# Kernel tuning notes

Hardware: AMD Instinct MI355X
Metric: run time of the kernel (lower is better)

Reference implementation:

```python
import jax, jax.numpy as jnp
import numpy as np

DIM = 1024
NUM_HEADS = 16
HEAD_DIM = DIM // NUM_HEADS
FF = 4 * DIM
B, T, S = 8, 512, 4096


def setup_inputs() -> dict:
    key = jax.random.key(0)
    ks = jax.random.split(key, 14)
    sc = 1.0 / np.sqrt(DIM)
    inp = {
        "x": jax.random.normal(ks[0], (B, T, DIM), jnp.float32),
        "inp": jax.random.normal(ks[1], (B, S, DIM), jnp.float32),
        # attention projections
        "Wq": jax.random.normal(ks[2], (DIM, DIM), jnp.float32) * sc,
        "bq": jnp.zeros((DIM,), jnp.float32),
        "Wk": jax.random.normal(ks[3], (DIM, DIM), jnp.float32) * sc,
        "bk": jnp.zeros((DIM,), jnp.float32),
        "Wv": jax.random.normal(ks[4], (DIM, DIM), jnp.float32) * sc,
        "bv": jnp.zeros((DIM,), jnp.float32),
        "Wo": jax.random.normal(ks[5], (DIM, DIM), jnp.float32) * sc,
        "bo": jnp.zeros((DIM,), jnp.float32),
        # MLP
        "W1": jax.random.normal(ks[6], (DIM, FF), jnp.float32) * sc,
        "b1": jnp.zeros((FF,), jnp.float32),
        "W2": jax.random.normal(ks[7], (FF, DIM), jnp.float32) * (1.0 / np.sqrt(FF)),
        "b2": jnp.zeros((DIM,), jnp.float32),
    }
    return inp


def _perceiver_layer(x, inp, Wq, bq, Wk, bk, Wv, bv, Wo, bo, W1, b1, W2, b2):
    b, t, _ = x.shape
    s = inp.shape[1]
    q = (x @ Wq + bq).reshape(b, t, NUM_HEADS, HEAD_DIM)
    k = (inp @ Wk + bk).reshape(b, s, NUM_HEADS, HEAD_DIM)
    v = (inp @ Wv + bv).reshape(b, s, NUM_HEADS, HEAD_DIM)
    # [b, h, t, s] score tensor (as in original code)
    attn = jnp.einsum('bthd,bshd->bhts', q, k)
    attn = jax.nn.softmax(attn / jnp.sqrt(jnp.float32(HEAD_DIM)), axis=-1)
    out = jnp.einsum('bhts,bshd->bthd', attn, v).reshape(b, t, DIM)
    attn_out = out @ Wo + bo
    x = x + attn_out
    h = jax.nn.gelu(x @ W1 + b1, approximate=True)  # flax nn.gelu default is tanh approx
    x = x + (h @ W2 + b2)
    return x


def reference(x, inp, Wq, bq, Wk, bk, Wv, bv, Wo, bo, W1, b1, W2, b2):
    return _perceiver_layer(x, inp, Wq, bq, Wk, bk, Wv, bv, Wo, bo, W1, b1, W2, b2)
```

## Files before the change

kernel.cpp:

```cpp
#include <hip/hip_runtime.h>
#include <hip/hip_bf16.h>

#define DIM 1024
#define NHEADS 16
#define HDIM 64
#define FF_ 4096
#define BB 8
#define TT 512
#define SS 4096

typedef __attribute__((ext_vector_type(8))) __bf16 bf16x8;
typedef __attribute__((ext_vector_type(4))) float f32x4;
typedef __attribute__((ext_vector_type(4))) unsigned short us4;

#define SWZ(r, b) ((b) ^ (((r) & 7) << 4))

typedef const __attribute__((address_space(1))) void gvoid_t;
typedef __attribute__((address_space(3))) void lvoid_t;

__device__ __forceinline__ void ldst16(const void* g, void* l) {
  __builtin_amdgcn_global_load_lds((gvoid_t*)g, (lvoid_t*)l, 16, 0, 0);
}

__device__ inline unsigned short f2bf(float f) {
  unsigned u = __float_as_uint(f);
  u += 0x7fff + ((u >> 16) & 1);
  return (unsigned short)(u >> 16);
}

__device__ __forceinline__ unsigned cvt_pk(float lo, float hi) {
  unsigned r;
  asm("v_cvt_pk_bf16_f32 %0, %1, %2" : "=v"(r) : "v"(lo), "v"(hi));
  return r;
}

__global__ void prep_kernel(const float* __restrict__ x,
                            const float* __restrict__ inp,
                            const float* __restrict__ Wq,
                            const float* __restrict__ Wk,
                            const float* __restrict__ Wv,
                            const float* __restrict__ Wo,
                            const float* __restrict__ W1,
                            const float* __restrict__ W2,
                            const float* __restrict__ bk,
                            const float* __restrict__ bv,
                            unsigned short* __restrict__ xb,
                            unsigned short* __restrict__ inpb,
                            unsigned short* __restrict__ Wqt,
                            unsigned short* __restrict__ Wkvt,
                            unsigned short* __restrict__ Wot,
                            unsigned short* __restrict__ W1t,
                            unsigned short* __restrict__ W2t,
                            float* __restrict__ bkv) {
  __shared__ float tile[32][33];
  const int bid = blockIdx.x, tid = threadIdx.x;

  if (bid < 2048) {
    const int n4 = BB * SS * DIM / 4;
    for (int i = bid * 256 + tid; i < n4; i += 2048 * 256) {
      float4 v = ((const float4*)inp)[i];
      uint2 w = {cvt_pk(v.x, v.y), cvt_pk(v.z, v.w)};
      ((uint2*)inpb)[i] = w;
    }
    return;
  }
  if (bid < 2304) {
    const int n4 = BB * TT * DIM / 4;
    for (int i = (bid - 2048) * 256 + tid; i < n4; i += 256 * 256) {
      float4 v = ((const float4*)x)[i];
      uint2 w = {cvt_pk(v.x, v.y), cvt_pk(v.z, v.w)};
      ((uint2*)xb)[i] = w;
    }
    return;
  }
  if (bid < 14592) {
    const float* in;
    unsigned short* outp;
    int R, C, t, tilesx;
    if (bid < 3328)       { in = Wq; outp = Wqt; R = 1024; C = 1024; t = bid - 2304; tilesx = 32; }
    else if (bid < 4352)  { in = Wk; outp = Wkvt; R = 1024; C = 1024; t = bid - 3328; tilesx = 32; }
    else if (bid < 5376)  { in = Wv; outp = Wkvt + 1024 * 1024; R = 1024; C = 1024; t = bid - 4352; tilesx = 32; }
    else if (bid < 6400)  { in = Wo; outp = Wot; R = 1024; C = 1024; t = bid - 5376; tilesx = 32; }
    else if (bid < 10496) { in = W1; outp = W1t; R = 1024; C = 4096; t = bid - 6400; tilesx = 128; }
    else                  { in = W2; outp = W2t; R = 4096; C = 1024; t = bid - 10496; tilesx = 32; }
    int bc = (t % tilesx) * 32, br = (t / tilesx) * 32;
    int tx = tid & 31, ty = tid >> 5;
#pragma unroll
    for (int i = 0; i < 32; i += 8)
      tile[ty + i][tx] = in[(size_t)(br + ty + i) * C + bc + tx];
    __syncthreads();
#pragma unroll
    for (int i = 0; i < 32; i += 8)
      outp[(size_t)(bc + ty + i) * R + br + tx] = f2bf(tile[tx][ty + i]);
    return;
  }
  for (int i = tid; i < 1024; i += 256) {
    bkv[i] = bk[i];
    bkv[1024 + i] = bv[i];
  }
}

template <int EPI>
__global__ __launch_bounds__(256, 3)
void gemm_kernel(const unsigned short* __restrict__ A,
                 const unsigned short* __restrict__ Bt,
                 const float* __restrict__ bias,
                 const float* __restrict__ res,
                 void* __restrict__ Cp,
                 unsigned short* __restrict__ C2,
                 int M, int N, int K) {
  __shared__ char smem[32768];
  char* As = smem;
  char* Bs = smem + 16384;

  const int tid = threadIdx.x;
  const int lane = tid & 63;
  const int wave = tid >> 6;
  const int wm = wave >> 1, wn = wave & 1;

  const int flat = blockIdx.y * gridDim.x + blockIdx.x;
  const int cpx = (gridDim.x * gridDim.y) >> 3;
  const int swz = (flat & 7) * cpx + (flat >> 3);
  const int m0 = (swz / gridDim.x) * 128, n0 = (swz % gridDim.x) * 128;

  f32x4 acc[4][4];
#pragma unroll
  for (int i = 0; i < 4; ++i)
#pragma unroll
    for (int j = 0; j < 4; ++j) acc[i][j] = (f32x4){0.f, 0.f, 0.f, 0.f};

  for (int k0 = 0; k0 < K; k0 += 64) {
    __syncthreads();
#pragma unroll
    for (int i = 0; i < 4; ++i) {
      int ch = (wave * 4 + i) * 64 + lane;
      int r = ch >> 3, c8 = (ch & 7) ^ (r & 7);
      ldst16(A + (size_t)(m0 + r) * K + k0 + c8 * 8, As + (wave * 4 + i) * 1024);
      ldst16(Bt + (size_t)(n0 + r) * K + k0 + c8 * 8, Bs + (wave * 4 + i) * 1024);
    }
    __syncthreads();

#pragma unroll
    for (int kk = 0; kk < 2; ++kk) {
      bf16x8 a[4], b[4];
#pragma unroll
      for (int mi = 0; mi < 4; ++mi) {
        int r = wm * 64 + mi * 16 + (lane & 15);
        a[mi] = *(const bf16x8*)(As + r * 128 + SWZ(r, kk * 64 + (lane >> 4) * 16));
      }
#pragma unroll
      for (int ni = 0; ni < 4; ++ni) {
        int r = wn * 64 + ni * 16 + (lane & 15);
        b[ni] = *(const bf16x8*)(Bs + r * 128 + SWZ(r, kk * 64 + (lane >> 4) * 16));
      }
#pragma unroll
      for (int mi = 0; mi < 4; ++mi)
#pragma unroll
        for (int ni = 0; ni < 4; ++ni)
          acc[mi][ni] = __builtin_amdgcn_mfma_f32_16x16x32_bf16(b[ni], a[mi], acc[mi][ni], 0, 0, 0);
    }
  }

  const int q = lane & 15, g4 = (lane >> 4) * 4;
#pragma unroll
  for (int mi = 0; mi < 4; ++mi) {
    int row = m0 + wm * 64 + mi * 16 + q;
#pragma unroll
    for (int ni = 0; ni < 4; ++ni) {
      int colb = n0 + wn * 64 + ni * 16 + g4;
      float4 bv = *(const float4*)(bias + colb);
      f32x4 v = acc[mi][ni];
      float v0 = v[0] + bv.x, v1 = v[1] + bv.y, v2 = v[2] + bv.z, v3 = v[3] + bv.w;
      if (EPI == 0) {
        uint2 w = {cvt_pk(v0, v1), cvt_pk(v2, v3)};
        *(uint2*)((unsigned short*)Cp + (size_t)row * N + colb) = w;
      } else if (EPI == 1) {
        float o[4] = {v0, v1, v2, v3};
#pragma unroll
        for (int j = 0; j < 4; ++j) {
          float u = 0.7978845608028654f * (o[j] + 0.044715f * o[j] * o[j] * o[j]);
          float e = __expf(2.f * u);
          float th = 1.f - 2.f / (e + 1.f);
          o[j] = 0.5f * o[j] * (1.f + th);
        }
        uint2 w = {cvt_pk(o[0], o[1]), cvt_pk(o[2], o[3])};
        *(uint2*)((unsigned short*)Cp + (size_t)row * N + colb) = w;
      } else {
        float4 r4 = *(const float4*)(res + (size_t)row * N + colb);
        float o0 = v0 + r4.x, o1 = v1 + r4.y, o2 = v2 + r4.z, o3 = v3 + r4.w;
        float4 ov = {o0, o1, o2, o3};
        *(float4*)((float*)Cp + (size_t)row * N + colb) = ov;
        if (EPI == 3) {
          uint2 w = {cvt_pk(o0, o1), cvt_pk(o2, o3)};
          *(uint2*)(C2 + (size_t)row * N + colb) = w;
        }
      }
    }
  }
}

template <int EPI>
__global__ __launch_bounds__(512, 2)
void gemm256(const unsigned short* __restrict__ A,
             const unsigned short* __restrict__ Bt,
             const float* __restrict__ bias,
             void* __restrict__ Cp,
             unsigned short* __restrict__ C2,
             int M, int N, int K) {
  __shared__ char smem[131072];

  const int tid = threadIdx.x, lane = tid & 63, wave = tid >> 6;
  const int q = lane & 15, g = lane >> 4;
  const int wm = wave >> 2, wn = wave & 3;

  const int flat = blockIdx.y * gridDim.x + blockIdx.x;
  const int cpx = (gridDim.x * gridDim.y) >> 3;
  const int swz = (flat & 7) * cpx + (flat >> 3);
  const int m0 = (swz / gridDim.x) * 256, n0 = (swz % gridDim.x) * 256;

  const unsigned short* Arow = A + (size_t)m0 * K;
  const unsigned short* Brow = Bt + (size_t)n0 * K;

  const int r0 = tid >> 3, c0 = ((tid & 7) ^ (r0 & 7)) * 8;
  const int r1 = (tid + 512) >> 3, c1 = (((tid + 512) & 7) ^ (r1 & 7)) * 8;

#define STA(buf, half, kt)                                                     \
  { char* d = smem + (buf) * 32768 + (half) * 16384;                           \
    const unsigned short* s = Arow + (size_t)((half) * 128) * K + (kt) * 64;   \
    ldst16(s + (size_t)r0 * K + c0, d + tid * 16);                             \
    ldst16(s + (size_t)r1 * K + c1, d + 8192 + tid * 16); }
#define STB(buf, half, kt)                                                     \
  { char* d = smem + 65536 + (buf) * 32768 + (half) * 16384;                   \
    const unsigned short* s = Brow + (size_t)((half) * 128) * K + (kt) * 64;   \
    ldst16(s + (size_t)r0 * K + c0, d + tid * 16);                             \
    ldst16(s + (size_t)r1 * K + c1, d + 8192 + tid * 16); }

  f32x4 acc[8][4];
#pragma unroll
  for (int i = 0; i < 8; ++i)
#pragma unroll
    for (int j = 0; j < 4; ++j) acc[i][j] = (f32x4){0.f, 0.f, 0.f, 0.f};

  STA(0, 0, 0); STA(0, 1, 0); STB(0, 0, 0); STB(0, 1, 0);
  STB(1, 0, 1); STB(1, 1, 1);
  asm volatile("s_waitcnt vmcnt(4)" ::: "memory");
  __builtin_amdgcn_s_barrier();

  const int NKT = K >> 6;
  for (int kt = 0; kt < NKT; ++kt) {
    const int cb = kt & 1, nb = cb ^ 1;
    const char* Ab = smem + cb * 32768;
    const char* Bb = smem + 65536 + cb * 32768;
    bf16x8 bfr[4][2];

#pragma unroll
    for (int p = 0; p < 4; ++p) {
      bf16x8 af[2][2];
#pragma unroll
      for (int i = 0; i < 2; ++i)
#pragma unroll
        for (int kk = 0; kk < 2; ++kk) {
          int r = wm * 128 + (2 * p + i) * 16 + q;
          af[i][kk] = *(const bf16x8*)(Ab + r * 128 + SWZ(r, kk * 64 + g * 16));
        }
      if (p == 0) {
#pragma unroll
        for (int nr = 0; nr < 4; ++nr)
#pragma unroll
          for (int kk = 0; kk < 2; ++kk) {
            int r = wn * 64 + nr * 16 + q;
            bfr[nr][kk] = *(const bf16x8*)(Bb + r * 128 + SWZ(r, kk * 64 + g * 16));
          }
      }

      if (p == 0)      { if (kt + 1 < NKT) { STA(nb, 0, kt + 1); STA(nb, 1, kt + 1); } }
      else if (p == 1) { if (kt + 2 < NKT) STB(cb, 0, kt + 2); }
      else if (p == 2) { if (kt + 2 < NKT) STB(cb, 1, kt + 2); }

      __builtin_amdgcn_s_barrier();
      __builtin_amdgcn_s_setprio(1);
#pragma unroll
      for (int i = 0; i < 2; ++i)
#pragma unroll
        for (int nr = 0; nr < 4; ++nr)
#pragma unroll
          for (int kk = 0; kk < 2; ++kk)
            acc[2 * p + i][nr] = __builtin_amdgcn_mfma_f32_16x16x32_bf16(
                bfr[nr][kk], af[i][kk], acc[2 * p + i][nr], 0, 0, 0);
      __builtin_amdgcn_s_setprio(0);

      if (p == 3) {
        if (kt + 2 < NKT) { asm volatile("s_waitcnt vmcnt(4)" ::: "memory"); }
        else              { asm volatile("s_waitcnt vmcnt(0)" ::: "memory"); }
      }
      __builtin_amdgcn_s_barrier();
    }
  }

  const int g4 = g * 4;
#pragma unroll
  for (int mr = 0; mr < 8; ++mr) {
    int row = m0 + wm * 128 + mr * 16 + q;
#pragma unroll
    for (int nr = 0; nr < 4; ++nr) {
      int colb = n0 + wn * 64 + nr * 16 + g4;
      float4 bv = *(const float4*)(bias + colb);
      f32x4 v = acc[mr][nr];
      float v0 = v[0] + bv.x, v1 = v[1] + bv.y, v2 = v[2] + bv.z, v3 = v[3] + bv.w;
      if (EPI == 1) {
        float o[4] = {v0, v1, v2, v3};
#pragma unroll
        for (int j = 0; j < 4; ++j) {
          float u = 0.7978845608028654f * (o[j] + 0.044715f * o[j] * o[j] * o[j]);
          float e = __expf(2.f * u);
          float th = 1.f - 2.f / (e + 1.f);
          o[j] = 0.5f * o[j] * (1.f + th);
        }
        uint2 w = {cvt_pk(o[0], o[1]), cvt_pk(o[2], o[3])};
        *(uint2*)((unsigned short*)Cp + (size_t)row * N + colb) = w;
      } else {
        if (n0 < 1024) {
          uint2 w = {cvt_pk(v0, v1), cvt_pk(v2, v3)};
          *(uint2*)((unsigned short*)Cp + (size_t)row * 1024 + colb) = w;
        } else {
          int b = row >> 12, s = row & 4095;
          int d0 = colb - 1024;
          unsigned short* vt = C2 + ((size_t)b * DIM + d0) * SS + s;
          vt[0] = f2bf(v0);
          vt[SS] = f2bf(v1);
          vt[2 * SS] = f2bf(v2);
          vt[3 * SS] = f2bf(v3);
        }
      }
    }
  }
#undef STA
#undef STB
}

__global__ __launch_bounds__(512, 4)
void attn_kernel4(const unsigned short* __restrict__ Qb,
                  const unsigned short* __restrict__ Kb,
                  const unsigned short* __restrict__ Vt,
                  unsigned short* __restrict__ Ob) {
  __shared__ char smem[81920];

  const int tid = threadIdx.x, lane = tid & 63, wave = tid >> 6;
  const int bid = blockIdx.x;
  const int b = bid & 7, qt = (bid >> 3) & 3, h = bid >> 5;
  const int q0 = qt * 128;
  const int q = lane & 15, g = lane >> 4;

  const int rK = tid >> 3;
  const int cK = (tid & 7) ^ (rK & 7);
  char* const Pw = smem + 65536 + wave * 2048;

  const unsigned short* srcQ = Qb + ((size_t)b * TT + q0) * DIM + h * HDIM;
  const unsigned short* srcK = Kb + (size_t)b * SS * DIM + h * HDIM;
  const unsigned short* srcV = Vt + ((size_t)b * DIM + h * HDIM) * SS;

  {
    int r = tid >> 3, c = (tid & 7) ^ (r & 7);
    ldst16(srcQ + (size_t)r * DIM + c * 8, smem + tid * 16);
    int ch = tid + 512;
    r = ch >> 3; c = (ch & 7) ^ (r & 7);
    ldst16(srcQ + (size_t)r * DIM + c * 8, smem + ch * 16);
  }
  ldst16(srcK + (size_t)rK * DIM + cK * 8, smem + 16384 + tid * 16);
  ldst16(srcV + (size_t)rK * SS + cK * 8, smem + 40960 + tid * 16);
  ldst16(srcK + (size_t)(64 + rK) * DIM + cK * 8, smem + 24576 + tid * 16);
  ldst16(srcV + (size_t)rK * SS + 64 + cK * 8, smem + 49152 + tid * 16);
  asm volatile("s_waitcnt vmcnt(2)" ::: "memory");
  __builtin_amdgcn_s_barrier();

  bf16x8 qf[2];
  {
    int r = wave * 16 + q;
    qf[0] = *(const bf16x8*)(smem + r * 128 + SWZ(r, g * 16));
    qf[1] = *(const bf16x8*)(smem + r * 128 + SWZ(r, 64 + g * 16));
  }

  f32x4 acc[4];
#pragma unroll
  for (int dt = 0; dt < 4; ++dt) acc[dt] = (f32x4){0.f, 0.f, 0.f, 0.f};
  float lsum = 0.f;
  const float CSC = 0.125f * 1.4426950408889634f;

  const int NT = SS / 64;
  int cur = 0, sb = 2;
  for (int t = 0; t < NT; ++t) {
    char* Kc = smem + 16384 + cur * 8192;
    char* Vc = smem + 40960 + cur * 8192;
    if (t + 2 < NT) {
      char* Kn = smem + 16384 + sb * 8192;
      char* Vn = smem + 40960 + sb * 8192;
      ldst16(srcK + (size_t)((t + 2) * 64 + rK) * DIM + cK * 8, Kn + tid * 16);
      ldst16(srcV + (size_t)rK * SS + (t + 2) * 64 + cK * 8, Vn + tid * 16);
    }

    f32x4 st[4];
#pragma unroll
    for (int si = 0; si < 4; ++si) st[si] = (f32x4){0.f, 0.f, 0.f, 0.f};
#pragma unroll
    for (int kk = 0; kk < 2; ++kk)
#pragma unroll
      for (int si = 0; si < 4; ++si) {
        int r = si * 16 + q;
        bf16x8 kf = *(const bf16x8*)(Kc + r * 128 + SWZ(r, kk * 64 + g * 16));
        st[si] = __builtin_amdgcn_mfma_f32_16x16x32_bf16(kf, qf[kk], st[si], 0, 0, 0);
      }

    float rs = 0.f;
#pragma unroll
    for (int si = 0; si < 4; ++si) {
      float p0 = __builtin_amdgcn_exp2f(st[si][0] * CSC);
      float p1 = __builtin_amdgcn_exp2f(st[si][1] * CSC);
      float p2 = __builtin_amdgcn_exp2f(st[si][2] * CSC);
      float p3 = __builtin_amdgcn_exp2f(st[si][3] * CSC);
      rs += (p0 + p1) + (p2 + p3);
      uint2 w = {cvt_pk(p0, p1), cvt_pk(p2, p3)};
      *(uint2*)(Pw + q * 128 + SWZ(q, si * 32 + g * 8)) = w;
    }
    lsum += rs;

#pragma unroll
    for (int kk = 0; kk < 2; ++kk) {
      bf16x8 pb = *(const bf16x8*)(Pw + q * 128 + SWZ(q, kk * 64 + g * 16));
#pragma unroll
      for (int dt = 0; dt < 4; ++dt) {
        int r = dt * 16 + q;
        bf16x8 va = *(const bf16x8*)(Vc + r * 128 + SWZ(r, kk * 64 + g * 16));
        acc[dt] = __builtin_amdgcn_mfma_f32_16x16x32_bf16(va, pb, acc[dt], 0, 0, 0);
      }
    }

    if (t + 2 < NT) { asm volatile("s_waitcnt vmcnt(2)" ::: "memory"); }
    else            { asm volatile("s_waitcnt vmcnt(0)" ::: "memory"); }
    __builtin_amdgcn_s_barrier();
    cur = cur == 2 ? 0 : cur + 1;
    sb  = sb  == 2 ? 0 : sb  + 1;
  }

  lsum += __shfl_xor(lsum, 16);
  lsum += __shfl_xor(lsum, 32);
  float inv = 1.0f / lsum;
#pragma unroll
  for (int dt = 0; dt < 4; ++dt) {
    f32x4 v = acc[dt];
    uint2 w = {cvt_pk(v[0] * inv, v[1] * inv), cvt_pk(v[2] * inv, v[3] * inv)};
    *(uint2*)(Pw + q * 128 + SWZ(q, dt * 32 + g * 8)) = w;
  }
  __builtin_amdgcn_s_waitcnt(0);
  int qr = lane >> 2, cb = (lane & 3) * 32;
  uint4 lo = *(const uint4*)(Pw + qr * 128 + SWZ(qr, cb));
  uint4 hi = *(const uint4*)(Pw + qr * 128 + SWZ(qr, cb + 16));
  size_t ob = ((size_t)b * TT + q0 + wave * 16 + qr) * DIM + h * HDIM + (lane & 3) * 16;
  *(uint4*)(Ob + ob) = lo;
  *(uint4*)(Ob + ob + 8) = hi;
}

extern "C" void kernel_launch(void* const* d_in, const int* in_sizes, int n_in,
                              void* d_out, int out_size, void* d_ws, size_t ws_size,
                              hipStream_t stream) {
  const float* x   = (const float*)d_in[0];
  const float* inp = (const float*)d_in[1];
  const float* Wq  = (const float*)d_in[2];
  const float* bq  = (const float*)d_in[3];
  const float* Wk  = (const float*)d_in[4];
  const float* bk  = (const float*)d_in[5];
  const float* Wv  = (const float*)d_in[6];
  const float* bv  = (const float*)d_in[7];
  const float* Wo  = (const float*)d_in[8];
  const float* bo  = (const float*)d_in[9];
  const float* W1  = (const float*)d_in[10];
  const float* b1  = (const float*)d_in[11];
  const float* W2  = (const float*)d_in[12];
  const float* b2  = (const float*)d_in[13];
  float* out = (float*)d_out;

  char* ws = (char*)d_ws;
  const size_t MB = 1024ull * 1024ull;
  unsigned short* Wqt  = (unsigned short*)(ws + 0 * MB);
  unsigned short* Wkvt = (unsigned short*)(ws + 2 * MB);
  unsigned short* Wot  = (unsigned short*)(ws + 6 * MB);
  unsigned short* W1t  = (unsigned short*)(ws + 8 * MB);
  unsigned short* W2t  = (unsigned short*)(ws + 16 * MB);
  float*          bkv  = (float*)(ws + 24 * MB);
  unsigned short* Qb   = (unsigned short*)(ws + 25 * MB);
  unsigned short* Kb   = (unsigned short*)(ws + 33 * MB);
  float*          x2   = (float*)(ws + 33 * MB);
  unsigned short* x2b  = (unsigned short*)(ws + 49 * MB);
  unsigned short* hb   = (unsigned short*)(ws + 57 * MB);
  unsigned short* Vt   = (unsigned short*)(ws + 97 * MB);
  unsigned short* inpb = (unsigned short*)(ws + 161 * MB);
  unsigned short* xb   = (unsigned short*)(ws + 225 * MB);
  unsigned short* Obf  = (unsigned short*)d_out;

  prep_kernel<<<dim3(14593), 256, 0, stream>>>(x, inp, Wq, Wk, Wv, Wo, W1, W2,
                                               bk, bv, xb, inpb, Wqt, Wkvt,
                                               Wot, W1t, W2t, bkv);

  gemm_kernel<0><<<dim3(8, 32), 256, 0, stream>>>(xb, Wqt, bq, nullptr, Qb, nullptr, BB * TT, DIM, DIM);
  gemm256<2><<<dim3(8, 128), 512, 0, stream>>>(inpb, Wkvt, bkv, Kb, Vt, BB * SS, 2048, DIM);

  attn_kernel4<<<dim3(512), 512, 0, stream>>>(Qb, Kb, Vt, Obf);

  gemm_kernel<3><<<dim3(8, 32), 256, 0, stream>>>(Obf, Wot, bo, x, x2, x2b, BB * TT, DIM, DIM);
  gemm256<1><<<dim3(16, 16), 512, 0, stream>>>(x2b, W1t, b1, hb, nullptr, BB * TT, FF_, DIM);
  gemm_kernel<2><<<dim3(8, 32), 256, 0, stream>>>(hb, W2t, b2, x2, out, nullptr, BB * TT, DIM, FF_);
}
```

Measured before the change: 458.7 us.

## Prefetch GEMM fragments across phases and shrink attention LDS footprint

In gemm256 the A/B register fragments for the next phase (and the next k-tile) are now read from LDS after the current MFMAs, so LDS reads overlap with compute instead of stalling before it. The vmcnt wait is moved earlier to p==2 so the next buffer is ready for the cross-tile prefetch. In the attention kernel Q is loaded directly from global memory into registers instead of being staged through LDS, cutting shared memory from 80KB to 64KB, which may allow more blocks per CU. The cost is higher register pressure in the GEMM, and uncoalesced direct global Q loads.

```diff
diff --git a/kernel.cpp b/kernel.cpp
--- a/kernel.cpp
+++ b/kernel.cpp
@@ -246,38 +246,37 @@
   asm volatile("s_waitcnt vmcnt(4)" ::: "memory");
   __builtin_amdgcn_s_barrier();
 
+  bf16x8 af[2][2], bfr[4][2];
+#pragma unroll
+  for (int i = 0; i < 2; ++i)
+#pragma unroll
+    for (int kk = 0; kk < 2; ++kk) {
+      int r = wm * 128 + i * 16 + q;
+      af[i][kk] = *(const bf16x8*)(smem + r * 128 + SWZ(r, kk * 64 + g * 16));
+    }
+#pragma unroll
+  for (int nr = 0; nr < 4; ++nr)
+#pragma unroll
+    for (int kk = 0; kk < 2; ++kk) {
+      int r = wn * 64 + nr * 16 + q;
+      bfr[nr][kk] = *(const bf16x8*)(smem + 65536 + r * 128 + SWZ(r, kk * 64 + g * 16));
+    }
+
   const int NKT = K >> 6;
   for (int kt = 0; kt < NKT; ++kt) {
     const int cb = kt & 1, nb = cb ^ 1;
     const char* Ab = smem + cb * 32768;
-    const char* Bb = smem + 65536 + cb * 32768;
-    bf16x8 bfr[4][2];
+    const char* An = smem + nb * 32768;
+    const char* Bn = smem + 65536 + nb * 32768;
 
 #pragma unroll
     for (int p = 0; p < 4; ++p) {
-      bf16x8 af[2][2];
-#pragma unroll
-      for (int i = 0; i < 2; ++i)
-#pragma unroll
-        for (int kk = 0; kk < 2; ++kk) {
-          int r = wm * 128 + (2 * p + i) * 16 + q;
-          af[i][kk] = *(const bf16x8*)(Ab + r * 128 + SWZ(r, kk * 64 + g * 16));
-        }
-      if (p == 0) {
-#pragma unroll
-        for (int nr = 0; nr < 4; ++nr)
-#pragma unroll
-          for (int kk = 0; kk < 2; ++kk) {
-            int r = wn * 64 + nr * 16 + q;
-            bfr[nr][kk] = *(const bf16x8*)(Bb + r * 128 + SWZ(r, kk * 64 + g * 16));
-          }
-      }
-
       if (p == 0)      { if (kt + 1 < NKT) { STA(nb, 0, kt + 1); STA(nb, 1, kt + 1); } }
       else if (p == 1) { if (kt + 2 < NKT) STB(cb, 0, kt + 2); }
       else if (p == 2) { if (kt + 2 < NKT) STB(cb, 1, kt + 2); }
 
       __builtin_amdgcn_s_barrier();
+
       __builtin_amdgcn_s_setprio(1);
 #pragma unroll
       for (int i = 0; i < 2; ++i)
@@ -289,11 +288,51 @@
                 bfr[nr][kk], af[i][kk], acc[2 * p + i][nr], 0, 0, 0);
       __builtin_amdgcn_s_setprio(0);
 
-      if (p == 3) {
+      bf16x8 afn[2][2], bfrn[4][2];
+      const bool have_next = (p < 3) || (kt + 1 < NKT);
+      if (p < 3) {
+#pragma unroll
+        for (int i = 0; i < 2; ++i)
+#pragma unroll
+          for (int kk = 0; kk < 2; ++kk) {
+            int r = wm * 128 + (2 * (p + 1) + i) * 16 + q;
+            afn[i][kk] = *(const bf16x8*)(Ab + r * 128 + SWZ(r, kk * 64 + g * 16));
+          }
+      } else if (kt + 1 < NKT) {
+#pragma unroll
+        for (int i = 0; i < 2; ++i)
+#pragma unroll
+          for (int kk = 0; kk < 2; ++kk) {
+            int r = wm * 128 + i * 16 + q;
+            afn[i][kk] = *(const bf16x8*)(An + r * 128 + SWZ(r, kk * 64 + g * 16));
+          }
+#pragma unroll
+        for (int nr = 0; nr < 4; ++nr)
+#pragma unroll
+          for (int kk = 0; kk < 2; ++kk) {
+            int r = wn * 64 + nr * 16 + q;
+            bfrn[nr][kk] = *(const bf16x8*)(Bn + r * 128 + SWZ(r, kk * 64 + g * 16));
+          }
+      }
+
+      if (p == 2) {
         if (kt + 2 < NKT) { asm volatile("s_waitcnt vmcnt(4)" ::: "memory"); }
         else              { asm volatile("s_waitcnt vmcnt(0)" ::: "memory"); }
       }
       __builtin_amdgcn_s_barrier();
+
+      if (have_next) {
+#pragma unroll
+        for (int i = 0; i < 2; ++i)
+#pragma unroll
+          for (int kk = 0; kk < 2; ++kk) af[i][kk] = afn[i][kk];
+        if (p == 3) {
+#pragma unroll
+          for (int nr = 0; nr < 4; ++nr)
+#pragma unroll
+            for (int kk = 0; kk < 2; ++kk) bfr[nr][kk] = bfrn[nr][kk];
+        }
+      }
     }
   }
 
@@ -339,11 +378,11 @@
 }
 
 __global__ __launch_bounds__(512, 4)
-void attn_kernel4(const unsigned short* __restrict__ Qb,
+void attn_kernel5(const unsigned short* __restrict__ Qb,
                   const unsigned short* __restrict__ Kb,
                   const unsigned short* __restrict__ Vt,
                   unsigned short* __restrict__ Ob) {
-  __shared__ char smem[81920];
+  __shared__ char smem[65536];
 
   const int tid = threadIdx.x, lane = tid & 63, wave = tid >> 6;
   const int bid = blockIdx.x;
@@ -353,32 +392,25 @@
 
   const int rK = tid >> 3;
   const int cK = (tid & 7) ^ (rK & 7);
-  char* const Pw = smem + 65536 + wave * 2048;
+  char* const Pw = smem + 49152 + wave * 2048;
 
   const unsigned short* srcQ = Qb + ((size_t)b * TT + q0) * DIM + h * HDIM;
   const unsigned short* srcK = Kb + (size_t)b * SS * DIM + h * HDIM;
   const unsigned short* srcV = Vt + ((size_t)b * DIM + h * HDIM) * SS;
 
+  bf16x8 qf[2];
   {
-    int r = tid >> 3, c = (tid & 7) ^ (r & 7);
-    ldst16(srcQ + (size_t)r * DIM + c * 8, smem + tid * 16);
-    int ch = tid + 512;
-    r = ch >> 3; c = (ch & 7) ^ (r & 7);
-    ldst16(srcQ + (size_t)r * DIM + c * 8, smem + ch * 16);
-  }
-  ldst16(srcK + (size_t)rK * DIM + cK * 8, smem + 16384 + tid * 16);
-  ldst16(srcV + (size_t)rK * SS + cK * 8, smem + 40960 + tid * 16);
-  ldst16(srcK + (size_t)(64 + rK) * DIM + cK * 8, smem + 24576 + tid * 16);
-  ldst16(srcV + (size_t)rK * SS + 64 + cK * 8, smem + 49152 + tid * 16);
+    const unsigned short* qrow = srcQ + (size_t)(wave * 16 + q) * DIM;
+    qf[0] = *(const bf16x8*)(qrow + g * 8);
+    qf[1] = *(const bf16x8*)(qrow + 32 + g * 8);
+  }
+
+  ldst16(srcK + (size_t)rK * DIM + cK * 8, smem + tid * 16);
+  ldst16(srcV + (size_t)rK * SS + cK * 8, smem + 24576 + tid * 16);
+  ldst16(srcK + (size_t)(64 + rK) * DIM + cK * 8, smem + 8192 + tid * 16);
+  ldst16(srcV + (size_t)rK * SS + 64 + cK * 8, smem + 32768 + tid * 16);
   asm volatile("s_waitcnt vmcnt(2)" ::: "memory");
   __builtin_amdgcn_s_barrier();
-
-  bf16x8 qf[2];
-  {
-    int r = wave * 16 + q;
-    qf[0] = *(const bf16x8*)(smem + r * 128 + SWZ(r, g * 16));
-    qf[1] = *(const bf16x8*)(smem + r * 128 + SWZ(r, 64 + g * 16));
-  }
 
   f32x4 acc[4];
 #pragma unroll
@@ -389,11 +421,11 @@
   const int NT = SS / 64;
   int cur = 0, sb = 2;
   for (int t = 0; t < NT; ++t) {
-    char* Kc = smem + 16384 + cur * 8192;
-    char* Vc = smem + 40960 + cur * 8192;
+    char* Kc = smem + cur * 8192;
+    char* Vc = smem + 24576 + cur * 8192;
     if (t + 2 < NT) {
-      char* Kn = smem + 16384 + sb * 8192;
-      char* Vn = smem + 40960 + sb * 8192;
+      char* Kn = smem + sb * 8192;
+      char* Vn = smem + 24576 + sb * 8192;
       ldst16(srcK + (size_t)((t + 2) * 64 + rK) * DIM + cK * 8, Kn + tid * 16);
       ldst16(srcV + (size_t)rK * SS + (t + 2) * 64 + cK * 8, Vn + tid * 16);
     }
@@ -503,7 +535,7 @@
   gemm_kernel<0><<<dim3(8, 32), 256, 0, stream>>>(xb, Wqt, bq, nullptr, Qb, nullptr, BB * TT, DIM, DIM);
   gemm256<2><<<dim3(8, 128), 512, 0, stream>>>(inpb, Wkvt, bkv, Kb, Vt, BB * SS, 2048, DIM);
 
-  attn_kernel4<<<dim3(512), 512, 0, stream>>>(Qb, Kb, Vt, Obf);
+  attn_kernel5<<<dim3(512), 512, 0, stream>>>(Qb, Kb, Vt, Obf);
 
   gemm_kernel<3><<<dim3(8, 32), 256, 0, stream>>>(Obf, Wot, bo, x, x2, x2b, BB * TT, DIM, DIM);
   gemm256<1><<<dim3(16, 16), 512, 0, stream>>>(x2b, W1t, b1, hb, nullptr, BB * TT, FF_, DIM);
```

Result: slower. 476.0 us (+3.8%).

## Give each attention wave two query tiles to reuse K/V fragments

Applied to the files above, without the earlier changes.

The attention kernel now runs 4 waves of 256 threads per block, each wave handling 32 query rows (two 16-row MFMA tiles) instead of 16. Each K and V fragment read from LDS therefore feeds two MFMAs, halving LDS reads per flop, and Q is loaded straight from global memory into registers rather than staged through shared memory. s_setprio is raised around the MFMA sections to favour matrix issue. The cost is more accumulator registers per wave and fewer waves per block to hide latency, with shared memory cut from 80KB to 64KB.

```diff
diff --git a/kernel.cpp b/kernel.cpp
--- a/kernel.cpp
+++ b/kernel.cpp
@@ -338,12 +338,12 @@
 #undef STB
 }
 
-__global__ __launch_bounds__(512, 4)
-void attn_kernel4(const unsigned short* __restrict__ Qb,
+__global__ __launch_bounds__(256, 2)
+void attn_kernel6(const unsigned short* __restrict__ Qb,
                   const unsigned short* __restrict__ Kb,
                   const unsigned short* __restrict__ Vt,
                   unsigned short* __restrict__ Ob) {
-  __shared__ char smem[81920];
+  __shared__ char smem[65536];
 
   const int tid = threadIdx.x, lane = tid & 63, wave = tid >> 6;
   const int bid = blockIdx.x;
@@ -351,112 +351,146 @@
   const int q0 = qt * 128;
   const int q = lane & 15, g = lane >> 4;
 
-  const int rK = tid >> 3;
-  const int cK = (tid & 7) ^ (rK & 7);
-  char* const Pw = smem + 65536 + wave * 2048;
+  const int rA = tid >> 3;
+  const int cA = (tid & 7) ^ (rA & 7);
+  char* const Pw = smem + 49152 + wave * 4096;
 
   const unsigned short* srcQ = Qb + ((size_t)b * TT + q0) * DIM + h * HDIM;
   const unsigned short* srcK = Kb + (size_t)b * SS * DIM + h * HDIM;
   const unsigned short* srcV = Vt + ((size_t)b * DIM + h * HDIM) * SS;
 
+  bf16x8 qf0[2], qf1[2];
   {
-    int r = tid >> 3, c = (tid & 7) ^ (r & 7);
-    ldst16(srcQ + (size_t)r * DIM + c * 8, smem + tid * 16);
-    int ch = tid + 512;
-    r = ch >> 3; c = (ch & 7) ^ (r & 7);
-    ldst16(srcQ + (size_t)r * DIM + c * 8, smem + ch * 16);
-  }
-  ldst16(srcK + (size_t)rK * DIM + cK * 8, smem + 16384 + tid * 16);
-  ldst16(srcV + (size_t)rK * SS + cK * 8, smem + 40960 + tid * 16);
-  ldst16(srcK + (size_t)(64 + rK) * DIM + cK * 8, smem + 24576 + tid * 16);
-  ldst16(srcV + (size_t)rK * SS + 64 + cK * 8, smem + 49152 + tid * 16);
-  asm volatile("s_waitcnt vmcnt(2)" ::: "memory");
+    const unsigned short* qr0 = srcQ + (size_t)(wave * 32 + q) * DIM;
+    const unsigned short* qr1 = srcQ + (size_t)(wave * 32 + 16 + q) * DIM;
+    qf0[0] = *(const bf16x8*)(qr0 + g * 8);
+    qf0[1] = *(const bf16x8*)(qr0 + 32 + g * 8);
+    qf1[0] = *(const bf16x8*)(qr1 + g * 8);
+    qf1[1] = *(const bf16x8*)(qr1 + 32 + g * 8);
+  }
+
+#define STKV(t, buf)                                                                        \
+  { ldst16(srcK + (size_t)((t) * 64 + rA) * DIM + cA * 8, smem + (buf) * 8192 + tid * 16);  \
+    ldst16(srcK + (size_t)((t) * 64 + rA + 32) * DIM + cA * 8,                              \
+           smem + (buf) * 8192 + 4096 + tid * 16);                                          \
+    ldst16(srcV + (size_t)rA * SS + (t) * 64 + cA * 8,                                      \
+           smem + 24576 + (buf) * 8192 + tid * 16);                                         \
+    ldst16(srcV + (size_t)(rA + 32) * SS + (t) * 64 + cA * 8,                               \
+           smem + 24576 + (buf) * 8192 + 4096 + tid * 16); }
+
+  STKV(0, 0);
+  STKV(1, 1);
+  asm volatile("s_waitcnt vmcnt(4)" ::: "memory");
   __builtin_amdgcn_s_barrier();
 
-  bf16x8 qf[2];
-  {
-    int r = wave * 16 + q;
-    qf[0] = *(const bf16x8*)(smem + r * 128 + SWZ(r, g * 16));
-    qf[1] = *(const bf16x8*)(smem + r * 128 + SWZ(r, 64 + g * 16));
-  }
-
-  f32x4 acc[4];
-#pragma unroll
-  for (int dt = 0; dt < 4; ++dt) acc[dt] = (f32x4){0.f, 0.f, 0.f, 0.f};
-  float lsum = 0.f;
+  f32x4 acc0[4], acc1[4];
+#pragma unroll
+  for (int dt = 0; dt < 4; ++dt) {
+    acc0[dt] = (f32x4){0.f, 0.f, 0.f, 0.f};
+    acc1[dt] = (f32x4){0.f, 0.f, 0.f, 0.f};
+  }
+  float lsum0 = 0.f, lsum1 = 0.f;
   const float CSC = 0.125f * 1.4426950408889634f;
 
   const int NT = SS / 64;
   int cur = 0, sb = 2;
   for (int t = 0; t < NT; ++t) {
-    char* Kc = smem + 16384 + cur * 8192;
-    char* Vc = smem + 40960 + cur * 8192;
-    if (t + 2 < NT) {
-      char* Kn = smem + 16384 + sb * 8192;
-      char* Vn = smem + 40960 + sb * 8192;
-      ldst16(srcK + (size_t)((t + 2) * 64 + rK) * DIM + cK * 8, Kn + tid * 16);
-      ldst16(srcV + (size_t)rK * SS + (t + 2) * 64 + cK * 8, Vn + tid * 16);
-    }
-
-    f32x4 st[4];
-#pragma unroll
-    for (int si = 0; si < 4; ++si) st[si] = (f32x4){0.f, 0.f, 0.f, 0.f};
+    char* Kc = smem + cur * 8192;
+    char* Vc = smem + 24576 + cur * 8192;
+    if (t + 2 < NT) STKV(t + 2, sb);
+
+    f32x4 st0[4], st1[4];
+#pragma unroll
+    for (int si = 0; si < 4; ++si) {
+      st0[si] = (f32x4){0.f, 0.f, 0.f, 0.f};
+      st1[si] = (f32x4){0.f, 0.f, 0.f, 0.f};
+    }
+    __builtin_amdgcn_s_setprio(1);
 #pragma unroll
     for (int kk = 0; kk < 2; ++kk)
 #pragma unroll
       for (int si = 0; si < 4; ++si) {
         int r = si * 16 + q;
         bf16x8 kf = *(const bf16x8*)(Kc + r * 128 + SWZ(r, kk * 64 + g * 16));
-        st[si] = __builtin_amdgcn_mfma_f32_16x16x32_bf16(kf, qf[kk], st[si], 0, 0, 0);
-      }
-
-    float rs = 0.f;
+        st0[si] = __builtin_amdgcn_mfma_f32_16x16x32_bf16(kf, qf0[kk], st0[si], 0, 0, 0);
+        st1[si] = __builtin_amdgcn_mfma_f32_16x16x32_bf16(kf, qf1[kk], st1[si], 0, 0, 0);
+      }
+    __builtin_amdgcn_s_setprio(0);
+
+    float rs0 = 0.f, rs1 = 0.f;
 #pragma unroll
     for (int si = 0; si < 4; ++si) {
-      float p0 = __builtin_amdgcn_exp2f(st[si][0] * CSC);
-      float p1 = __builtin_amdgcn_exp2f(st[si][1] * CSC);
-      float p2 = __builtin_amdgcn_exp2f(st[si][2] * CSC);
-      float p3 = __builtin_amdgcn_exp2f(st[si][3] * CSC);
-      rs += (p0 + p1) + (p2 + p3);
-      uint2 w = {cvt_pk(p0, p1), cvt_pk(p2, p3)};
-      *(uint2*)(Pw + q * 128 + SWZ(q, si * 32 + g * 8)) = w;
-    }
-    lsum += rs;
-
+      float a0 = __builtin_amdgcn_exp2f(st0[si][0] * CSC);
+      float a1 = __builtin_amdgcn_exp2f(st0[si][1] * CSC);
+      float a2 = __builtin_amdgcn_exp2f(st0[si][2] * CSC);
+      float a3 = __builtin_amdgcn_exp2f(st0[si][3] * CSC);
+      rs0 += (a0 + a1) + (a2 + a3);
+      uint2 w0 = {cvt_pk(a0, a1), cvt_pk(a2, a3)};
+      *(uint2*)(Pw + q * 128 + SWZ(q, si * 32 + g * 8)) = w0;
+      float b0 = __builtin_amdgcn_exp2f(st1[si][0] * CSC);
+      float b1 = __builtin_amdgcn_exp2f(st1[si][1] * CSC);
+      float b2 = __builtin_amdgcn_exp2f(st1[si][2] * CSC);
+      float b3 = __builtin_amdgcn_exp2f(st1[si][3] * CSC);
+      rs1 += (b0 + b1) + (b2 + b3);
+      uint2 w1 = {cvt_pk(b0, b1), cvt_pk(b2, b3)};
+      *(uint2*)(Pw + 2048 + q * 128 + SWZ(q, si * 32 + g * 8)) = w1;
+    }
+    lsum0 += rs0;
+    lsum1 += rs1;
+
+    __builtin_amdgcn_s_setprio(1);
 #pragma unroll
     for (int kk = 0; kk < 2; ++kk) {
-      bf16x8 pb = *(const bf16x8*)(Pw + q * 128 + SWZ(q, kk * 64 + g * 16));
+      bf16x8 pb0 = *(const bf16x8*)(Pw + q * 128 + SWZ(q, kk * 64 + g * 16));
+      bf16x8 pb1 = *(const bf16x8*)(Pw + 2048 + q * 128 + SWZ(q, kk * 64 + g * 16));
 #pragma unroll
       for (int dt = 0; dt < 4; ++dt) {
         int r = dt * 16 + q;
         bf16x8 va = *(const bf16x8*)(Vc + r * 128 + SWZ(r, kk * 64 + g * 16));
-        acc[dt] = __builtin_amdgcn_mfma_f32_16x16x32_bf16(va, pb, acc[dt], 0, 0, 0);
-      }
-    }
-
-    if (t + 2 < NT) { asm volatile("s_waitcnt vmcnt(2)" ::: "memory"); }
+        acc0[dt] = __builtin_amdgcn_mfma_f32_16x16x32_bf16(va, pb0, acc0[dt], 0, 0, 0);
+        acc1[dt] = __builtin_amdgcn_mfma_f32_16x16x32_bf16(va, pb1, acc1[dt], 0, 0, 0);
+      }
+    }
+    __builtin_amdgcn_s_setprio(0);
+
+    if (t + 2 < NT) { asm volatile("s_waitcnt vmcnt(4)" ::: "memory"); }
     else            { asm volatile("s_waitcnt vmcnt(0)" ::: "memory"); }
     __builtin_amdgcn_s_barrier();
     cur = cur == 2 ? 0 : cur + 1;
     sb  = sb  == 2 ? 0 : sb  + 1;
   }
-
-  lsum += __shfl_xor(lsum, 16);
-  lsum += __shfl_xor(lsum, 32);
-  float inv = 1.0f / lsum;
+#undef STKV
+
+  lsum0 += __shfl_xor(lsum0, 16);
+  lsum0 += __shfl_xor(lsum0, 32);
+  lsum1 += __shfl_xor(lsum1, 16);
+  lsum1 += __shfl_xor(lsum1, 32);
+  float inv0 = 1.0f / lsum0, inv1 = 1.0f / lsum1;
 #pragma unroll
   for (int dt = 0; dt < 4; ++dt) {
-    f32x4 v = acc[dt];
-    uint2 w = {cvt_pk(v[0] * inv, v[1] * inv), cvt_pk(v[2] * inv, v[3] * inv)};
-    *(uint2*)(Pw + q * 128 + SWZ(q, dt * 32 + g * 8)) = w;
+    f32x4 v0 = acc0[dt];
+    uint2 w0 = {cvt_pk(v0[0] * inv0, v0[1] * inv0), cvt_pk(v0[2] * inv0, v0[3] * inv0)};
+    *(uint2*)(Pw + q * 128 + SWZ(q, dt * 32 + g * 8)) = w0;
+    f32x4 v1 = acc1[dt];
+    uint2 w1 = {cvt_pk(v1[0] * inv1, v1[1] * inv1), cvt_pk(v1[2] * inv1, v1[3] * inv1)};
+    *(uint2*)(Pw + 2048 + q * 128 + SWZ(q, dt * 32 + g * 8)) = w1;
   }
   __builtin_amdgcn_s_waitcnt(0);
   int qr = lane >> 2, cb = (lane & 3) * 32;
-  uint4 lo = *(const uint4*)(Pw + qr * 128 + SWZ(qr, cb));
-  uint4 hi = *(const uint4*)(Pw + qr * 128 + SWZ(qr, cb + 16));
-  size_t ob = ((size_t)b * TT + q0 + wave * 16 + qr) * DIM + h * HDIM + (lane & 3) * 16;
-  *(uint4*)(Ob + ob) = lo;
-  *(uint4*)(Ob + ob + 8) = hi;
+  {
+    uint4 lo = *(const uint4*)(Pw + qr * 128 + SWZ(qr, cb));
+    uint4 hi = *(const uint4*)(Pw + qr * 128 + SWZ(qr, cb + 16));
+    size_t ob = ((size_t)b * TT + q0 + wave * 32 + qr) * DIM + h * HDIM + (lane & 3) * 16;
+    *(uint4*)(Ob + ob) = lo;
+    *(uint4*)(Ob + ob + 8) = hi;
+  }
+  {
+    uint4 lo = *(const uint4*)(Pw + 2048 + qr * 128 + SWZ(qr, cb));
+    uint4 hi = *(const uint4*)(Pw + 2048 + qr * 128 + SWZ(qr, cb + 16));
+    size_t ob = ((size_t)b * TT + q0 + wave * 32 + 16 + qr) * DIM + h * HDIM + (lane & 3) * 16;
+    *(uint4*)(Ob + ob) = lo;
+    *(uint4*)(Ob + ob + 8) = hi;
+  }
 }
 
 extern "C" void kernel_launch(void* const* d_in, const int* in_sizes, int n_in,
@@ -503,7 +537,7 @@
   gemm_kernel<0><<<dim3(8, 32), 256, 0, stream>>>(xb, Wqt, bq, nullptr, Qb, nullptr, BB * TT, DIM, DIM);
   gemm256<2><<<dim3(8, 128), 512, 0, stream>>>(inpb, Wkvt, bkv, Kb, Vt, BB * SS, 2048, DIM);
 
-  attn_kernel4<<<dim3(512), 512, 0, stream>>>(Qb, Kb, Vt, Obf);
+  attn_kernel6<<<dim3(512), 256, 0, stream>>>(Qb, Kb, Vt, Obf);
 
   gemm_kernel<3><<<dim3(8, 32), 256, 0, stream>>>(Obf, Wot, bo, x, x2, x2b, BB * TT, DIM, DIM);
   gemm256<1><<<dim3(16, 16), 512, 0, stream>>>(x2b, W1t, b1, hb, nullptr, BB * TT, FF_, DIM);
```

Measured after the change: 452.7 us, median of 2. No clear change (-1.3%).
